# Performance work log

Hardware: AMD Instinct MI355X
Metric: run time of the kernel (lower is better)

The kernel has to match this reference:

```python
import jax, jax.numpy as jnp
import numpy as np

E, D, H, T = 8, 1024, 4096, 8192  # num_expert, d_model, d_hidden, total_tokens


def setup_inputs() -> dict:
    key = jax.random.key(0)
    k1, k2, k3, k4, k5 = jax.random.split(key, 5)
    inp = jax.random.normal(k1, (T, D), dtype=jnp.float32)
    # FMoELinear weights: [E, out_features, in_features], bias [E, out_features]
    w1 = jax.random.normal(k2, (E, H, D), dtype=jnp.float32) * 0.02
    b1 = jax.random.normal(k3, (E, H), dtype=jnp.float32) * 0.02
    w2 = jax.random.normal(k4, (E, D, H), dtype=jnp.float32) * 0.02
    b2 = jax.random.normal(k5, (E, D), dtype=jnp.float32) * 0.02
    # tokens are contiguous per expert; equal split here (counts may vary in general)
    fwd_expert_count = jnp.full((E,), T // E, dtype=jnp.int32)
    return {"inp": inp, "w1": w1, "b1": b1, "w2": w2, "b2": b2,
            "fwd_expert_count": fwd_expert_count}


def _expert_ids(counts, n_tokens):
    # token t belongs to expert e iff cumsum(counts)[e-1] <= t < cumsum(counts)[e]
    offsets = jnp.cumsum(counts)  # [E]
    t = jnp.arange(n_tokens)
    return jnp.sum(t[:, None] >= offsets[None, :], axis=1)  # [T] in [0, E]


def _grouped_linear(x, W, b, eid):
    # grouped GEMM: y[t] = W[eid[t]] @ x[t] + b[eid[t]]; tokens with eid >= E -> 0
    n_exp = W.shape[0]
    acc = jnp.zeros((x.shape[0], W.shape[1]), dtype=x.dtype)
    for e in range(n_exp):  # small fixed loop over experts
        ye = x @ W[e].T + b[e]
        acc = acc + jnp.where((eid == e)[:, None], ye, jnp.zeros((), x.dtype))
    return acc


def reference(inp, w1, b1, w2, b2, fwd_expert_count):
    eid = _expert_ids(fwd_expert_count, inp.shape[0])
    h = _grouped_linear(inp, w1, b1, eid)   # [T, H]
    h = jax.nn.gelu(h)
    out = _grouped_linear(h, w2, b2, eid)   # [T, D]
    return out
```

## Files before the change

kernel.cpp:

```cpp
#include <hip/hip_runtime.h>
#include <hip/hip_bf16.h>
#include <cstdint>
#include <cstddef>


using bf16 = __hip_bfloat16;
typedef __attribute__((ext_vector_type(8))) short bf16x8;
typedef __attribute__((ext_vector_type(4))) float f32x4;

#define BM 256
#define BN 128
#define BK 64

typedef const __attribute__((address_space(1))) unsigned int g_u32;
typedef __attribute__((address_space(3))) unsigned int l_u32;

__device__ __forceinline__ void async16(void* lds, const void* g) {
  __builtin_amdgcn_global_load_lds((g_u32*)g, (l_u32*)lds, 16, 0, 0);
}

__device__ __forceinline__ float gelu_f(float x) {
  const float c0 = 0.7978845608028654f;
  const float c1 = 0.044715f;
  float u = c0 * (x + c1 * x * x * x);
  float t = 1.0f - 2.0f / (__expf(2.0f * u) + 1.0f);
  return 0.5f * x * (1.0f + t);
}

__device__ __forceinline__ void cvt8(const float* in, bf16* out, size_t i) {
  f32x4 lo = *(const f32x4*)(in + i);
  f32x4 hi = *(const f32x4*)(in + i + 4);
  bf16 cv[8];
#pragma unroll
  for (int k = 0; k < 4; ++k) {
    cv[k]     = __float2bfloat16(lo[k]);
    cv[k + 4] = __float2bfloat16(hi[k]);
  }
  *(bf16x8*)(out + i) = *(const bf16x8*)cv;
}

__global__ __launch_bounds__(256) void f32_to_bf16_2(
    const float* __restrict__ a, bf16* __restrict__ oa, size_t na,
    const float* __restrict__ b, bf16* __restrict__ ob, size_t nb) {
  const size_t stride = (size_t)gridDim.x * blockDim.x * 8;
  const size_t base = ((size_t)blockIdx.x * blockDim.x + threadIdx.x) * 8;
  for (size_t i = base; i < na; i += stride) cvt8(a, oa, i);
  for (size_t i = base; i < nb; i += stride) cvt8(b, ob, i);
}

__global__ __launch_bounds__(256) void f32_to_bf16_3(
    const float* __restrict__ a, bf16* __restrict__ oa, size_t na,
    const float* __restrict__ b, bf16* __restrict__ ob, size_t nb,
    const float* __restrict__ c, bf16* __restrict__ oc, size_t nc) {
  const size_t stride = (size_t)gridDim.x * blockDim.x * 8;
  const size_t base = ((size_t)blockIdx.x * blockDim.x + threadIdx.x) * 8;
  for (size_t i = base; i < na; i += stride) cvt8(a, oa, i);
  for (size_t i = base; i < nb; i += stride) cvt8(b, ob, i);
  for (size_t i = base; i < nc; i += stride) cvt8(c, oc, i);
}

__global__ __launch_bounds__(512) void gemm_bt_bf16(
    const bf16* __restrict__ A,
    const bf16* __restrict__ B,
    const float* __restrict__ bias,
    void* __restrict__ Cv,
    const int* __restrict__ counts,
    int E, int N, int K, int c_is_bf16_gelu)
{
  __shared__ alignas(16) bf16 As[3][BM * BK];
  __shared__ alignas(16) bf16 Bs[3][BN * BK];

  const int tid  = threadIdx.x;
  const int lane = tid & 63;
  const int wave = tid >> 6;

  const int gx   = gridDim.x;
  const int nwg  = gx * gridDim.y;
  const int orig = blockIdx.y * gx + blockIdx.x;
  const int qq = nwg >> 3, rr = nwg & 7;
  const int xcd = orig & 7, lo = orig >> 3;
  const int wgid = (xcd < rr ? xcd * (qq + 1) : rr * (qq + 1) + (xcd - rr) * qq) + lo;
  const int m0 = (wgid / gx) * BM;
  const int n0 = (wgid % gx) * BN;

  int eid = 0;
  {
    long long cum = 0;
    for (int e = 0; e < E; ++e) { cum += counts[e]; if (m0 >= cum) eid = e + 1; }
  }

  const int wm = wave >> 1;
  const int wn = wave & 1;

  f32x4 acc[4][4] = {};

  if (eid < E) {
    const bf16* Ag = A + (size_t)m0 * K;
    const bf16* Bg = B + (size_t)eid * (size_t)N * (size_t)K + (size_t)n0 * K;

    const int rlane = wave * 8 + (lane >> 3);
    const int swz   = ((lane & 7) ^ ((lane >> 3) & 7)) * 8;

    const int abase = (wm * 64 + (lane & 15)) * BK;
    const int bbase = (wn * 64 + (lane & 15)) * BK;
    const int swzf0 = (((lane >> 4) + 0) ^ (lane & 7)) * 8;
    const int swzf1 = (((lane >> 4) + 4) ^ (lane & 7)) * 8;

    const int nt = K / BK;

    auto STAGE = [&](int bi, int kt) {
#pragma unroll
      for (int c = 0; c < 4; ++c)
        async16(&As[bi][c * 4096 + wave * 512],
                Ag + (size_t)(c * 64 + rlane) * K + kt + swz);
#pragma unroll
      for (int c = 0; c < 2; ++c)
        async16(&Bs[bi][c * 4096 + wave * 512],
                Bg + (size_t)(c * 64 + rlane) * K + kt + swz);
    };

    auto MMA = [&](const bf16* Ab, const bf16* Bb) {
#pragma unroll
      for (int ks = 0; ks < 2; ++ks) {
        const int sw = ks ? swzf1 : swzf0;
        bf16x8 a[4], b[4];
#pragma unroll
        for (int i = 0; i < 4; ++i)
          a[i] = *(const bf16x8*)&Ab[abase + i * 16 * BK + sw];
#pragma unroll
        for (int j = 0; j < 4; ++j)
          b[j] = *(const bf16x8*)&Bb[bbase + j * 16 * BK + sw];
#pragma unroll
        for (int i = 0; i < 4; ++i)
#pragma unroll
          for (int j = 0; j < 4; ++j)
            acc[i][j] = __builtin_amdgcn_mfma_f32_16x16x32_bf16(a[i], b[j], acc[i][j], 0, 0, 0);
      }
    };

    STAGE(0, 0);
    STAGE(1, BK);

    for (int t = 0; t < nt; ++t) {
      if (t < nt - 1) asm volatile("s_waitcnt vmcnt(6)" ::: "memory");
      else            asm volatile("s_waitcnt vmcnt(0)" ::: "memory");
      __builtin_amdgcn_s_barrier();
      if (t + 2 < nt) STAGE((t + 2) % 3, (t + 2) * BK);
      MMA(As[t % 3], Bs[t % 3]);
    }
  }

  const int crow = (lane >> 4) * 4;
  const int ccol = lane & 15;
  const int do_gelu = c_is_bf16_gelu;

  if (eid < E) {
    float bv[4];
#pragma unroll
    for (int j = 0; j < 4; ++j)
      bv[j] = bias[(size_t)eid * N + n0 + wn * 64 + j * 16 + ccol];
#pragma unroll
    for (int i = 0; i < 4; ++i) {
#pragma unroll
      for (int r = 0; r < 4; ++r) {
        size_t grow = (size_t)(m0 + wm * 64 + i * 16 + crow + r);
#pragma unroll
        for (int j = 0; j < 4; ++j) {
          float v = acc[i][j][r] + bv[j];
          size_t idx = grow * N + n0 + wn * 64 + j * 16 + ccol;
          if (do_gelu) ((bf16*)Cv)[idx] = __float2bfloat16(gelu_f(v));
          else         ((float*)Cv)[idx] = v;
        }
      }
    }
  } else {
#pragma unroll
    for (int i = 0; i < 4; ++i) {
#pragma unroll
      for (int r = 0; r < 4; ++r) {
        size_t grow = (size_t)(m0 + wm * 64 + i * 16 + crow + r);
#pragma unroll
        for (int j = 0; j < 4; ++j) {
          size_t idx = grow * N + n0 + wn * 64 + j * 16 + ccol;
          if (do_gelu) ((bf16*)Cv)[idx] = __float2bfloat16(0.0f);
          else         ((float*)Cv)[idx] = 0.0f;
        }
      }
    }
  }
}

#define FBM 128
#define FBK 32

__device__ __forceinline__ void stage_f32(const float* g, bf16* lds,
                                          int srow, int seg, int ldg) {
#pragma unroll
  for (int h = 0; h < 2; ++h) {
    const float* p = g + (size_t)(srow + h * 64) * ldg + seg;
    f32x4 lo = *(const f32x4*)(p);
    f32x4 hi = *(const f32x4*)(p + 4);
    bf16 cv[8];
#pragma unroll
    for (int i = 0; i < 4; ++i) {
      cv[i]     = __float2bfloat16(lo[i]);
      cv[i + 4] = __float2bfloat16(hi[i]);
    }
    *(bf16x8*)&lds[(srow + h * 64) * FBK + seg] = *(const bf16x8*)cv;
  }
}

__device__ __forceinline__ void stage_bf16f(const bf16* g, bf16* lds,
                                            int srow, int seg, int ldg) {
#pragma unroll
  for (int h = 0; h < 2; ++h) {
    const bf16* p = g + (size_t)(srow + h * 64) * ldg + seg;
    *(bf16x8*)&lds[(srow + h * 64) * FBK + seg] = *(const bf16x8*)p;
  }
}

template <bool AF32>
__global__ __launch_bounds__(256) void grouped_gemm_bt(
    const void* __restrict__ Av, const float* __restrict__ B,
    const float* __restrict__ bias, void* __restrict__ Cv,
    const int* __restrict__ counts, int E, int N, int K, int c_is_bf16_gelu)
{
  __shared__ alignas(16) bf16 As[FBM * FBK];
  __shared__ alignas(16) bf16 Bs[FBM * FBK];

  const int tid  = threadIdx.x;
  const int lane = tid & 63;
  const int wave = tid >> 6;
  const int m0 = blockIdx.y * FBM;
  const int n0 = blockIdx.x * FBM;

  int eid = 0;
  {
    long long cum = 0;
    for (int e = 0; e < E; ++e) { cum += counts[e]; if (m0 >= cum) eid = e + 1; }
  }

  const int wrow = (wave >> 1) * 64;
  const int wcol = (wave & 1) * 64;

  f32x4 acc[4][4] = {};

  if (eid < E) {
    const float* Bexp = B + (size_t)eid * (size_t)N * (size_t)K;
    const int srow = tid >> 2;
    const int seg  = (tid & 3) * 8;
    const int frow = lane & 15;
    const int fk   = (lane >> 4) * 8;

    for (int kt = 0; kt < K; kt += FBK) {
      if (AF32)
        stage_f32((const float*)Av + (size_t)(m0 + srow) * K + kt - (size_t)srow * K,
                  As, srow, seg, K);
      else
        stage_bf16f((const bf16*)Av + (size_t)(m0 + srow) * K + kt - (size_t)srow * K,
                    As, srow, seg, K);
      stage_f32(Bexp + (size_t)(n0 + srow) * K + kt - (size_t)srow * K,
                Bs, srow, seg, K);
      __syncthreads();

      bf16x8 af[4], bfr[4];
#pragma unroll
      for (int i = 0; i < 4; ++i)
        af[i] = *(const bf16x8*)&As[(wrow + i * 16 + frow) * FBK + fk];
#pragma unroll
      for (int j = 0; j < 4; ++j)
        bfr[j] = *(const bf16x8*)&Bs[(wcol + j * 16 + frow) * FBK + fk];

#pragma unroll
      for (int i = 0; i < 4; ++i)
#pragma unroll
        for (int j = 0; j < 4; ++j)
          acc[i][j] = __builtin_amdgcn_mfma_f32_16x16x32_bf16(af[i], bfr[j], acc[i][j], 0, 0, 0);

      __syncthreads();
    }
  }

  const int crow = (lane >> 4) * 4;
  const int ccol = lane & 15;
  const int do_gelu = c_is_bf16_gelu;

  if (eid < E) {
    float bv[4];
#pragma unroll
    for (int j = 0; j < 4; ++j)
      bv[j] = bias[(size_t)eid * N + n0 + wcol + j * 16 + ccol];
#pragma unroll
    for (int i = 0; i < 4; ++i) {
#pragma unroll
      for (int r = 0; r < 4; ++r) {
        size_t grow = (size_t)(m0 + wrow + i * 16 + crow + r);
#pragma unroll
        for (int j = 0; j < 4; ++j) {
          float v = acc[i][j][r] + bv[j];
          size_t idx = grow * N + n0 + wcol + j * 16 + ccol;
          if (do_gelu) ((bf16*)Cv)[idx] = __float2bfloat16(gelu_f(v));
          else         ((float*)Cv)[idx] = v;
        }
      }
    }
  } else {
#pragma unroll
    for (int i = 0; i < 4; ++i) {
#pragma unroll
      for (int r = 0; r < 4; ++r) {
        size_t grow = (size_t)(m0 + wrow + i * 16 + crow + r);
#pragma unroll
        for (int j = 0; j < 4; ++j) {
          size_t idx = grow * N + n0 + wcol + j * 16 + ccol;
          if (do_gelu) ((bf16*)Cv)[idx] = __float2bfloat16(0.0f);
          else         ((float*)Cv)[idx] = 0.0f;
        }
      }
    }
  }
}

extern "C" void kernel_launch(void* const* d_in, const int* in_sizes, int n_in,
                              void* d_out, int out_size, void* d_ws, size_t ws_size,
                              hipStream_t stream) {
  const float* inp = (const float*)d_in[0];
  const float* w1  = (const float*)d_in[1];
  const float* b1  = (const float*)d_in[2];
  const float* w2  = (const float*)d_in[3];
  const float* b2  = (const float*)d_in[4];
  const int* cnt   = (const int*)d_in[5];
  float* out = (float*)d_out;

  const int E = in_sizes[5];
  const int H = in_sizes[2] / E;
  const int D = in_sizes[4] / E;
  const int T = in_sizes[0] / D;

  const size_t szH = (size_t)T * H * sizeof(bf16);
  const size_t szX = (size_t)T * D * sizeof(bf16);
  const size_t szW = (size_t)E * (size_t)H * D * sizeof(bf16);

  const size_t nX = (size_t)T * D;
  const size_t nW = (size_t)E * (size_t)H * D;

  dim3 cblk(256), gblk(512);
  dim3 g1(H / BN, T / BM);
  dim3 g2(D / BN, T / BM);

  if (ws_size >= szH + szX + 2 * szW) {
    bf16* h   = (bf16*)d_ws;
    bf16* xb  = (bf16*)((char*)d_ws + szH);
    bf16* w1b = (bf16*)((char*)d_ws + szH + szX);
    bf16* w2b = (bf16*)((char*)d_ws + szH + szX + szW);

    f32_to_bf16_3<<<dim3(4096), cblk, 0, stream>>>(inp, xb, nX, w1, w1b, nW,
                                                   w2, w2b, nW);
    gemm_bt_bf16<<<g1, gblk, 0, stream>>>(xb, w1b, b1, h, cnt, E, H, D, 1);
    gemm_bt_bf16<<<g2, gblk, 0, stream>>>(h, w2b, b2, out, cnt, E, D, H, 0);
  } else if (ws_size >= szH + szX + szW) {
    bf16* h  = (bf16*)d_ws;
    bf16* xb = (bf16*)((char*)d_ws + szH);
    bf16* wb = (bf16*)((char*)d_ws + szH + szX);

    f32_to_bf16_2<<<dim3(2048), cblk, 0, stream>>>(inp, xb, nX, w1, wb, nW);
    gemm_bt_bf16<<<g1, gblk, 0, stream>>>(xb, wb, b1, h, cnt, E, H, D, 1);
    f32_to_bf16_2<<<dim3(2048), cblk, 0, stream>>>(w2, wb, nW, nullptr, nullptr, 0);
    gemm_bt_bf16<<<g2, gblk, 0, stream>>>(h, wb, b2, out, cnt, E, D, H, 0);
  } else {
    bf16* h = (bf16*)d_ws;
    grouped_gemm_bt<true><<<dim3(H / FBM, T / FBM), cblk, 0, stream>>>(
        inp, w1, b1, h, cnt, E, H, D, 1);
    grouped_gemm_bt<false><<<dim3(D / FBM, T / FBM), cblk, 0, stream>>>(
        h, w2, b2, out, cnt, E, D, H, 0);
  }
}
```

Baseline: 578.8 us.

## Use 256x256 tiles with 8-phase ping-pong schedule and split-K for second GEMM

Replaces the 256x128 triple-buffered GEMM with a 256x256 tile kernel whose double-buffered main loop interleaves quarter-tile LDS reads, async global loads and MFMA bursts under barriers and raised wave priority. The second GEMM is split along K in two, with partial sums added by float atomics into an output that the conversion kernel pre-fills with the expert bias. The aims are higher arithmetic intensity per tile and enough workgroups to fill the GPU for the narrow D=1024 GEMM. The costs are more accumulator registers (likely lower occupancy), atomic traffic, and non-deterministic summation order.

```diff
diff --git a/kernel.cpp b/kernel.cpp
--- a/kernel.cpp
+++ b/kernel.cpp
@@ -9,7 +9,7 @@
 typedef __attribute__((ext_vector_type(4))) float f32x4;
 
 #define BM 256
-#define BN 128
+#define BN 256
 #define BK 64
 
 typedef const __attribute__((address_space(1))) unsigned int g_u32;
@@ -39,40 +39,63 @@
   *(bf16x8*)(out + i) = *(const bf16x8*)cv;
 }
 
-__global__ __launch_bounds__(256) void f32_to_bf16_2(
-    const float* __restrict__ a, bf16* __restrict__ oa, size_t na,
-    const float* __restrict__ b, bf16* __restrict__ ob, size_t nb) {
-  const size_t stride = (size_t)gridDim.x * blockDim.x * 8;
-  const size_t base = ((size_t)blockIdx.x * blockDim.x + threadIdx.x) * 8;
-  for (size_t i = base; i < na; i += stride) cvt8(a, oa, i);
-  for (size_t i = base; i < nb; i += stride) cvt8(b, ob, i);
+__device__ __forceinline__ void bias_fill(float* out, const float* b2,
+    const int* counts, int E, int T, int D) {
+  for (int row = blockIdx.x; row < T; row += gridDim.x) {
+    int eid = 0;
+    long long cum = 0;
+    for (int e = 0; e < E; ++e) { cum += counts[e]; if (row >= cum) eid = e + 1; }
+    f32x4* dst = (f32x4*)(out + (size_t)row * D);
+    if (eid < E) {
+      const f32x4* src = (const f32x4*)(b2 + (size_t)eid * D);
+      for (int c = threadIdx.x; c < (D >> 2); c += blockDim.x) dst[c] = src[c];
+    } else {
+      const f32x4 z = {};
+      for (int c = threadIdx.x; c < (D >> 2); c += blockDim.x) dst[c] = z;
+    }
+  }
 }
 
 __global__ __launch_bounds__(256) void f32_to_bf16_3(
     const float* __restrict__ a, bf16* __restrict__ oa, size_t na,
     const float* __restrict__ b, bf16* __restrict__ ob, size_t nb,
-    const float* __restrict__ c, bf16* __restrict__ oc, size_t nc) {
+    const float* __restrict__ c, bf16* __restrict__ oc, size_t nc,
+    float* out, const float* b2, const int* counts, int E, int T, int D) {
   const size_t stride = (size_t)gridDim.x * blockDim.x * 8;
   const size_t base = ((size_t)blockIdx.x * blockDim.x + threadIdx.x) * 8;
   for (size_t i = base; i < na; i += stride) cvt8(a, oa, i);
   for (size_t i = base; i < nb; i += stride) cvt8(b, ob, i);
   for (size_t i = base; i < nc; i += stride) cvt8(c, oc, i);
-}
-
-__global__ __launch_bounds__(512) void gemm_bt_bf16(
+  if (out) bias_fill(out, b2, counts, E, T, D);
+}
+
+__global__ __launch_bounds__(256) void f32_to_bf16_2(
+    const float* __restrict__ a, bf16* __restrict__ oa, size_t na,
+    const float* __restrict__ b, bf16* __restrict__ ob, size_t nb,
+    float* out, const float* b2, const int* counts, int E, int T, int D) {
+  const size_t stride = (size_t)gridDim.x * blockDim.x * 8;
+  const size_t base = ((size_t)blockIdx.x * blockDim.x + threadIdx.x) * 8;
+  for (size_t i = base; i < na; i += stride) cvt8(a, oa, i);
+  if (b) for (size_t i = base; i < nb; i += stride) cvt8(b, ob, i);
+  if (out) bias_fill(out, b2, counts, E, T, D);
+}
+
+__global__ __launch_bounds__(512) void gemm8p(
     const bf16* __restrict__ A,
     const bf16* __restrict__ B,
     const float* __restrict__ bias,
     void* __restrict__ Cv,
     const int* __restrict__ counts,
-    int E, int N, int K, int c_is_bf16_gelu)
+    int E, int N, int K, int mode)
 {
-  __shared__ alignas(16) bf16 As[3][BM * BK];
-  __shared__ alignas(16) bf16 Bs[3][BN * BK];
+  __shared__ alignas(16) bf16 As[2][BM * BK];
+  __shared__ alignas(16) bf16 Bs[2][BN * BK];
 
   const int tid  = threadIdx.x;
   const int lane = tid & 63;
   const int wave = tid >> 6;
+  const int wm = wave >> 2;
+  const int wn = wave & 3;
 
   const int gx   = gridDim.x;
   const int nwg  = gx * gridDim.y;
@@ -83,107 +106,155 @@
   const int m0 = (wgid / gx) * BM;
   const int n0 = (wgid % gx) * BN;
 
+  const int klen = K / (int)gridDim.z;
+  const int k0 = blockIdx.z * klen;
+
   int eid = 0;
   {
     long long cum = 0;
     for (int e = 0; e < E; ++e) { cum += counts[e]; if (m0 >= cum) eid = e + 1; }
   }
 
-  const int wm = wave >> 1;
-  const int wn = wave & 1;
-
-  f32x4 acc[4][4] = {};
+  f32x4 acc[8][4] = {};
 
   if (eid < E) {
     const bf16* Ag = A + (size_t)m0 * K;
     const bf16* Bg = B + (size_t)eid * (size_t)N * (size_t)K + (size_t)n0 * K;
 
-    const int rlane = wave * 8 + (lane >> 3);
-    const int swz   = ((lane & 7) ^ ((lane >> 3) & 7)) * 8;
-
-    const int abase = (wm * 64 + (lane & 15)) * BK;
-    const int bbase = (wn * 64 + (lane & 15)) * BK;
-    const int swzf0 = (((lane >> 4) + 0) ^ (lane & 7)) * 8;
-    const int swzf1 = (((lane >> 4) + 4) ^ (lane & 7)) * 8;
-
-    const int nt = K / BK;
-
-    auto STAGE = [&](int bi, int kt) {
-#pragma unroll
-      for (int c = 0; c < 4; ++c)
-        async16(&As[bi][c * 4096 + wave * 512],
-                Ag + (size_t)(c * 64 + rlane) * K + kt + swz);
-#pragma unroll
-      for (int c = 0; c < 2; ++c)
-        async16(&Bs[bi][c * 4096 + wave * 512],
-                Bg + (size_t)(c * 64 + rlane) * K + kt + swz);
-    };
-
-    auto MMA = [&](const bf16* Ab, const bf16* Bb) {
-#pragma unroll
-      for (int ks = 0; ks < 2; ++ks) {
-        const int sw = ks ? swzf1 : swzf0;
-        bf16x8 a[4], b[4];
-#pragma unroll
-        for (int i = 0; i < 4; ++i)
-          a[i] = *(const bf16x8*)&Ab[abase + i * 16 * BK + sw];
-#pragma unroll
-        for (int j = 0; j < 4; ++j)
-          b[j] = *(const bf16x8*)&Bb[bbase + j * 16 * BK + sw];
-#pragma unroll
-        for (int i = 0; i < 4; ++i)
-#pragma unroll
-          for (int j = 0; j < 4; ++j)
-            acc[i][j] = __builtin_amdgcn_mfma_f32_16x16x32_bf16(a[i], b[j], acc[i][j], 0, 0, 0);
-      }
-    };
-
-    STAGE(0, 0);
-    STAGE(1, BK);
-
-    for (int t = 0; t < nt; ++t) {
-      if (t < nt - 1) asm volatile("s_waitcnt vmcnt(6)" ::: "memory");
-      else            asm volatile("s_waitcnt vmcnt(0)" ::: "memory");
-      __builtin_amdgcn_s_barrier();
-      if (t + 2 < nt) STAGE((t + 2) % 3, (t + 2) * BK);
-      MMA(As[t % 3], Bs[t % 3]);
-    }
+    const int swzcol = ((tid & 7) ^ ((tid >> 3) & 7)) * 8;
+
+    const int sk0 = (((lane >> 4) + 0) ^ (lane & 7)) * 16;
+    const int sk1 = (((lane >> 4) + 4) ^ (lane & 7)) * 16;
+    const int aBase = (wm * 128 + (lane & 15)) * 128;
+    const int bBase = (wn * 64  + (lane & 15)) * 128;
+
+    const int nt = klen / BK;
+
+    bf16x8 av[4][2], blo[2][2], bhi[2][2];
+
+#define RD_A(BUF, MI)                                                        \
+  { const char* _p = (const char*)&As[BUF][0] + aBase + (MI) * 8192;         \
+    _Pragma("unroll") for (int ii = 0; ii < 4; ++ii) {                       \
+      av[ii][0] = *(const bf16x8*)(_p + ii * 2048 + sk0);                    \
+      av[ii][1] = *(const bf16x8*)(_p + ii * 2048 + sk1); } }
+
+#define RD_B(BUF, HALF, BV)                                                  \
+  { const char* _p = (const char*)&Bs[BUF][0] + bBase + (HALF) * 4096;       \
+    _Pragma("unroll") for (int jj = 0; jj < 2; ++jj) {                       \
+      BV[jj][0] = *(const bf16x8*)(_p + jj * 2048 + sk0);                    \
+      BV[jj][1] = *(const bf16x8*)(_p + jj * 2048 + sk1); } }
+
+#define MMAQ(MI, HALF, BV)                                                   \
+  _Pragma("unroll") for (int ii = 0; ii < 4; ++ii)                           \
+  _Pragma("unroll") for (int jj = 0; jj < 2; ++jj)                           \
+  _Pragma("unroll") for (int ks = 0; ks < 2; ++ks)                           \
+    acc[(MI)*4 + ii][(HALF)*2 + jj] = __builtin_amdgcn_mfma_f32_16x16x32_bf16( \
+      av[ii][ks], BV[jj][ks], acc[(MI)*4 + ii][(HALF)*2 + jj], 0, 0, 0);
+
+#define ST_A(BUF, H, TI)                                                     \
+  { const int _kt = k0 + ((TI) < nt ? (TI) : nt - 1) * BK;                   \
+    _Pragma("unroll") for (int c = 0; c < 2; ++c) {                          \
+      const int _r = (H) * 64 + c * 128 + (tid >> 3);                        \
+      async16((char*)&As[BUF][0] + _r * 128 + (tid & 7) * 16,                \
+              Ag + (size_t)_r * K + _kt + swzcol); } }
+
+#define ST_B(BUF, H, TI)                                                     \
+  { const int _kt = k0 + ((TI) < nt ? (TI) : nt - 1) * BK;                   \
+    _Pragma("unroll") for (int c = 0; c < 2; ++c) {                          \
+      const int _u = c * 512 + tid;                                          \
+      const int _r = (H) * 32 + (_u >> 8) * 64 + ((_u >> 3) & 31);           \
+      async16((char*)&Bs[BUF][0] + _r * 128 + (tid & 7) * 16,                \
+              Bg + (size_t)_r * K + _kt + swzcol); } }
+
+#define BAR __builtin_amdgcn_s_barrier()
+#define VMC6 asm volatile("s_waitcnt vmcnt(6)" ::: "memory")
+#define PRIO1 __builtin_amdgcn_s_setprio(1)
+#define PRIO0 __builtin_amdgcn_s_setprio(0)
+
+    ST_A(0, 0, 0); ST_B(0, 0, 0); ST_A(0, 1, 0); ST_B(0, 1, 0);
+    ST_A(1, 0, 1); ST_B(1, 0, 1); ST_A(1, 1, 1);
+    VMC6; BAR;
+
+    for (int it = 0; it < nt / 2; ++it) {
+      const int a = 2 * it, b = a + 1;
+      RD_A(0, 0); RD_B(0, 0, blo); ST_B(1, 1, b);
+      BAR; PRIO1; MMAQ(0, 0, blo); PRIO0; BAR;
+      RD_B(0, 1, bhi); ST_A(0, 0, a + 2);
+      BAR; PRIO1; MMAQ(0, 1, bhi); PRIO0; BAR;
+      RD_A(0, 1); ST_B(0, 0, a + 2);
+      BAR; PRIO1; MMAQ(1, 1, bhi); PRIO0; BAR;
+      ST_A(0, 1, a + 2); VMC6;
+      BAR; PRIO1; MMAQ(1, 0, blo); PRIO0; BAR;
+      RD_A(1, 0); RD_B(1, 0, blo); ST_B(0, 1, a + 2);
+      BAR; PRIO1; MMAQ(0, 0, blo); PRIO0; BAR;
+      RD_B(1, 1, bhi); ST_A(1, 0, b + 2);
+      BAR; PRIO1; MMAQ(0, 1, bhi); PRIO0; BAR;
+      RD_A(1, 1); ST_B(1, 0, b + 2);
+      BAR; PRIO1; MMAQ(1, 1, bhi); PRIO0; BAR;
+      ST_A(1, 1, b + 2); VMC6;
+      BAR; PRIO1; MMAQ(1, 0, blo); PRIO0; BAR;
+    }
+    asm volatile("s_waitcnt vmcnt(0)" ::: "memory");
+
+#undef RD_A
+#undef RD_B
+#undef MMAQ
+#undef ST_A
+#undef ST_B
+#undef BAR
+#undef VMC6
+#undef PRIO1
+#undef PRIO0
   }
 
   const int crow = (lane >> 4) * 4;
   const int ccol = lane & 15;
-  const int do_gelu = c_is_bf16_gelu;
 
   if (eid < E) {
-    float bv[4];
-#pragma unroll
-    for (int j = 0; j < 4; ++j)
-      bv[j] = bias[(size_t)eid * N + n0 + wn * 64 + j * 16 + ccol];
-#pragma unroll
-    for (int i = 0; i < 4; ++i) {
-#pragma unroll
-      for (int r = 0; r < 4; ++r) {
-        size_t grow = (size_t)(m0 + wm * 64 + i * 16 + crow + r);
-#pragma unroll
-        for (int j = 0; j < 4; ++j) {
-          float v = acc[i][j][r] + bv[j];
-          size_t idx = grow * N + n0 + wn * 64 + j * 16 + ccol;
-          if (do_gelu) ((bf16*)Cv)[idx] = __float2bfloat16(gelu_f(v));
-          else         ((float*)Cv)[idx] = v;
+    if (mode == 2) {
+      float* outF = (float*)Cv;
+#pragma unroll
+      for (int i = 0; i < 8; ++i) {
+#pragma unroll
+        for (int r = 0; r < 4; ++r) {
+          const size_t grow = (size_t)(m0 + wm * 128 + i * 16 + crow + r);
+#pragma unroll
+          for (int j = 0; j < 4; ++j)
+            atomicAdd(&outF[grow * N + n0 + wn * 64 + j * 16 + ccol],
+                      acc[i][j][r]);
         }
       }
-    }
-  } else {
-#pragma unroll
-    for (int i = 0; i < 4; ++i) {
+    } else {
+      float bv[4];
+#pragma unroll
+      for (int j = 0; j < 4; ++j)
+        bv[j] = bias[(size_t)eid * N + n0 + wn * 64 + j * 16 + ccol];
+#pragma unroll
+      for (int i = 0; i < 8; ++i) {
+#pragma unroll
+        for (int r = 0; r < 4; ++r) {
+          const size_t grow = (size_t)(m0 + wm * 128 + i * 16 + crow + r);
+#pragma unroll
+          for (int j = 0; j < 4; ++j) {
+            const float v = acc[i][j][r] + bv[j];
+            const size_t idx = grow * N + n0 + wn * 64 + j * 16 + ccol;
+            if (mode == 1) ((bf16*)Cv)[idx] = __float2bfloat16(gelu_f(v));
+            else           ((float*)Cv)[idx] = v;
+          }
+        }
+      }
+    }
+  } else if (mode != 2) {
+#pragma unroll
+    for (int i = 0; i < 8; ++i) {
 #pragma unroll
       for (int r = 0; r < 4; ++r) {
-        size_t grow = (size_t)(m0 + wm * 64 + i * 16 + crow + r);
+        const size_t grow = (size_t)(m0 + wm * 128 + i * 16 + crow + r);
 #pragma unroll
         for (int j = 0; j < 4; ++j) {
-          size_t idx = grow * N + n0 + wn * 64 + j * 16 + ccol;
-          if (do_gelu) ((bf16*)Cv)[idx] = __float2bfloat16(0.0f);
-          else         ((float*)Cv)[idx] = 0.0f;
+          const size_t idx = grow * N + n0 + wn * 64 + j * 16 + ccol;
+          if (mode == 1) ((bf16*)Cv)[idx] = __float2bfloat16(0.0f);
+          else           ((float*)Cv)[idx] = 0.0f;
         }
       }
     }
@@ -344,29 +415,35 @@
   const size_t nX = (size_t)T * D;
   const size_t nW = (size_t)E * (size_t)H * D;
 
+  const int SPLITK = 2;
+  const bool ok8p = (T % BM == 0) && (H % BN == 0) && (D % BN == 0) &&
+                    (D % (2 * BK) == 0) && (H % (SPLITK * 2 * BK) == 0);
+
   dim3 cblk(256), gblk(512);
-  dim3 g1(H / BN, T / BM);
-  dim3 g2(D / BN, T / BM);
-
-  if (ws_size >= szH + szX + 2 * szW) {
+  dim3 g1(H / BN, T / BM, 1);
+  dim3 g2(D / BN, T / BM, SPLITK);
+
+  if (ok8p && ws_size >= szH + szX + 2 * szW) {
     bf16* h   = (bf16*)d_ws;
     bf16* xb  = (bf16*)((char*)d_ws + szH);
     bf16* w1b = (bf16*)((char*)d_ws + szH + szX);
     bf16* w2b = (bf16*)((char*)d_ws + szH + szX + szW);
 
-    f32_to_bf16_3<<<dim3(4096), cblk, 0, stream>>>(inp, xb, nX, w1, w1b, nW,
-                                                   w2, w2b, nW);
-    gemm_bt_bf16<<<g1, gblk, 0, stream>>>(xb, w1b, b1, h, cnt, E, H, D, 1);
-    gemm_bt_bf16<<<g2, gblk, 0, stream>>>(h, w2b, b2, out, cnt, E, D, H, 0);
-  } else if (ws_size >= szH + szX + szW) {
+    f32_to_bf16_3<<<dim3(4096), cblk, 0, stream>>>(
+        inp, xb, nX, w1, w1b, nW, w2, w2b, nW, out, b2, cnt, E, T, D);
+    gemm8p<<<g1, gblk, 0, stream>>>(xb, w1b, b1, h, cnt, E, H, D, 1);
+    gemm8p<<<g2, gblk, 0, stream>>>(h, w2b, b2, out, cnt, E, D, H, 2);
+  } else if (ok8p && ws_size >= szH + szX + szW) {
     bf16* h  = (bf16*)d_ws;
     bf16* xb = (bf16*)((char*)d_ws + szH);
     bf16* wb = (bf16*)((char*)d_ws + szH + szX);
 
-    f32_to_bf16_2<<<dim3(2048), cblk, 0, stream>>>(inp, xb, nX, w1, wb, nW);
-    gemm_bt_bf16<<<g1, gblk, 0, stream>>>(xb, wb, b1, h, cnt, E, H, D, 1);
-    f32_to_bf16_2<<<dim3(2048), cblk, 0, stream>>>(w2, wb, nW, nullptr, nullptr, 0);
-    gemm_bt_bf16<<<g2, gblk, 0, stream>>>(h, wb, b2, out, cnt, E, D, H, 0);
+    f32_to_bf16_2<<<dim3(2048), cblk, 0, stream>>>(
+        inp, xb, nX, w1, wb, nW, out, b2, cnt, E, T, D);
+    gemm8p<<<g1, gblk, 0, stream>>>(xb, wb, b1, h, cnt, E, H, D, 1);
+    f32_to_bf16_2<<<dim3(2048), cblk, 0, stream>>>(
+        w2, wb, nW, nullptr, nullptr, 0, nullptr, nullptr, nullptr, 0, 0, 0);
+    gemm8p<<<g2, gblk, 0, stream>>>(h, wb, b2, out, cnt, E, D, H, 2);
   } else {
     bf16* h = (bf16*)d_ws;
     grouped_gemm_bt<true><<<dim3(H / FBM, T / FBM), cblk, 0, stream>>>(
```

New measurement: 550.0 us. 1.05x faster.
